# Kernel tuning notes

Measured on AMD Instinct MI355X. Metric: run time of the kernel, lower is better.

## Reference

```python
import jax, jax.numpy as jnp
import numpy as np

B, S, D, H, FFN = 8, 1024, 1024, 16, 4096
DH = D // H  # per-head dim = 64
NEG = -1e9
EPS = 1e-5


def layer_norm(x):
    # F.layer_norm over last dim, no affine params (matches add_and_norm_dropout)
    mu = jnp.mean(x, axis=-1, keepdims=True)
    var = jnp.var(x, axis=-1, keepdims=True)
    return (x - mu) / jnp.sqrt(var + EPS)


def setup_inputs() -> dict:
    key = jax.random.key(0)
    ks = jax.random.split(key, 10)
    scale = 1.0 / np.sqrt(D)
    x = jax.random.normal(ks[0], (B, S, D), dtype=jnp.float32)
    real_lengths = jax.random.randint(ks[1], (B,), 1, S + 1)
    # per-head projection weights stacked: [H, D, DH] (nn.Linear(D, DH, bias=False) per head)
    Wq = jax.random.uniform(ks[2], (H, D, DH), jnp.float32, -scale, scale)
    Wk = jax.random.uniform(ks[3], (H, D, DH), jnp.float32, -scale, scale)
    Wv = jax.random.uniform(ks[4], (H, D, DH), jnp.float32, -scale, scale)
    Wo = jax.random.uniform(ks[5], (D, H * DH), jnp.float32, -scale, scale)  # Linear(H*DH, D, bias=False)
    W1 = jax.random.uniform(ks[6], (FFN, D), jnp.float32, -scale, scale)
    b1 = jax.random.uniform(ks[7], (FFN,), jnp.float32, -scale, scale)
    s2 = 1.0 / np.sqrt(FFN)
    W2 = jax.random.uniform(ks[8], (D, FFN), jnp.float32, -s2, s2)
    b2 = jax.random.uniform(ks[9], (D,), jnp.float32, -s2, s2)
    return {"x": x, "real_lengths": real_lengths, "Wq": Wq, "Wk": Wk, "Wv": Wv,
            "Wo": Wo, "W1": W1, "b1": b1, "W2": W2, "b2": b2}


def reference(x, real_lengths, Wq, Wk, Wv, Wo, W1, b1, W2, b2):
    b, s, d = x.shape
    # padding mask: True where key position >= real_length (masked out)
    key_pad = jnp.arange(s)[None, :] >= real_lengths[:, None]  # [B, S]

    # batched per-head projections (equivalent to the Python per-head loop)
    q = jnp.einsum('bsd,hde->bhse', x, Wq)
    k = jnp.einsum('bsd,hde->bhse', x, Wk)
    v = jnp.einsum('bsd,hde->bhse', x, Wv)

    scores = jnp.einsum('bhse,bhte->bhst', q, k) / jnp.sqrt(jnp.float32(DH))
    scores = jnp.where(key_pad[:, None, None, :], NEG, scores)
    attn = jax.nn.softmax(scores, axis=-1)
    heads = jnp.einsum('bhst,bhte->bhse', attn, v)       # [B,H,S,DH]
    concat = heads.transpose(0, 2, 1, 3).reshape(b, s, d)  # head concat
    attn_out = concat @ Wo.T

    x1 = layer_norm(x + attn_out)  # add & norm (eval: no dropout)

    ffn = jax.nn.relu(x1 @ W1.T + b1) @ W2.T + b2
    return layer_norm(x1 + ffn)
```

## Files before the change

### kernel.cpp

```cpp
#include <hip/hip_runtime.h>
#include <hip/hip_bf16.h>
#include <math.h>

#define B_ 8
#define S_ 1024
#define D_ 1024
#define H_ 16
#define DH_ 64
#define FFN_ 4096
#define NEG_ (-1e9f)
#define EPS_ 1e-5f

typedef float f32x4 __attribute__((ext_vector_type(4)));
typedef short bf16x8 __attribute__((ext_vector_type(8)));

__device__ __forceinline__ ushort f2b(float f) {
  __hip_bfloat16 h = __float2bfloat16(f);
  return *reinterpret_cast<ushort*>(&h);
}
__device__ __forceinline__ float b2f(ushort u) {
  return __uint_as_float((unsigned)u << 16);
}

__device__ __forceinline__ void gload16(const void* g, void* l) {
  auto* lp = (__attribute__((address_space(3))) unsigned*)(uintptr_t)(l);
  __builtin_amdgcn_global_load_lds(
      (const __attribute__((address_space(1))) unsigned*)g, lp, 16, 0, 0);
}

__device__ __forceinline__ void* swz_ptr(void* base, int row, int col) {
  int byte = (row << 7) + (col << 1);
  byte ^= (row & 7) << 4;
  return (char*)base + byte;
}
__device__ __forceinline__ void* swz256(void* base, int row, int col) {
  int byte = (row << 8) + (col << 1);
  byte ^= (row & 7) << 4;
  return (char*)base + byte;
}

#define BARR asm volatile("s_barrier" ::: "memory")
#define LGKM0                                         \
  do {                                                \
    asm volatile("s_waitcnt lgkmcnt(0)" ::: "memory"); \
    __builtin_amdgcn_sched_barrier(0);                \
  } while (0)

__global__ __launch_bounds__(256) void prep_k(
    const float* __restrict__ x, const float* __restrict__ Wq,
    const float* __restrict__ Wk, const float* __restrict__ Wv,
    const float* __restrict__ Wo, const float* __restrict__ W1,
    const float* __restrict__ W2, ushort* __restrict__ xbf,
    ushort* __restrict__ qkvw, ushort* __restrict__ wob,
    ushort* __restrict__ w1b, ushort* __restrict__ w2b) {
  const int blk = blockIdx.x, t = threadIdx.x;
  if (blk < 8192) {
    int i = blk * 256 + t;
    float4 v = ((const float4*)x)[i];
    ushort4 o;
    o.x = f2b(v.x); o.y = f2b(v.y); o.z = f2b(v.z); o.w = f2b(v.w);
    ((ushort4*)xbf)[i] = o;
  } else if (blk < 8192 + 12288) {
    int idx = (blk - 8192) * 256 + t;
    int e = idx & 63, k = (idx >> 6) & 1023;
    int h = (idx >> 16) & 15, which = idx >> 20;
    const float* W = (which == 0) ? Wq : (which == 1 ? Wk : Wv);
    float v = W[((size_t)h * D_ + k) * DH_ + e];
    qkvw[((size_t)which * 1024 + h * 64 + e) * 1024 + k] = f2b(v);
  } else if (blk < 8192 + 12288 + 1024) {
    int i = (blk - 8192 - 12288) * 256 + t;
    float4 v = ((const float4*)Wo)[i];
    ushort4 o;
    o.x = f2b(v.x); o.y = f2b(v.y); o.z = f2b(v.z); o.w = f2b(v.w);
    ((ushort4*)wob)[i] = o;
  } else if (blk < 8192 + 12288 + 1024 + 4096) {
    int i = (blk - 8192 - 12288 - 1024) * 256 + t;
    float4 v = ((const float4*)W1)[i];
    ushort4 o;
    o.x = f2b(v.x); o.y = f2b(v.y); o.z = f2b(v.z); o.w = f2b(v.w);
    ((ushort4*)w1b)[i] = o;
  } else {
    int i = (blk - 8192 - 12288 - 1024 - 4096) * 256 + t;
    float4 v = ((const float4*)W2)[i];
    ushort4 o;
    o.x = f2b(v.x); o.y = f2b(v.y); o.z = f2b(v.z); o.w = f2b(v.w);
    ((ushort4*)w2b)[i] = o;
  }
}

template <int BIAS, int RELU, int VSPLIT>
__global__ __launch_bounds__(512, 2) void gemm8p(
    const ushort* __restrict__ A, const ushort* __restrict__ Bt,
    const float* __restrict__ bias, ushort* __restrict__ C,
    ushort* __restrict__ vT, int M, int N, int K) {
  __shared__ ushort lds[2][2][2][256 * 32];
  const int nbn = N >> 8;
  const int nwg = gridDim.x;
  const int cpx = nwg >> 3;
  const int bid = blockIdx.x;
  const int swz = (bid & 7) * cpx + (bid >> 3);
  const int bm = swz / nbn, bn = swz % nbn;

  const int t = threadIdx.x;
  const int lane = t & 63, lr = lane & 15, lg = lane >> 4;
  const int wid = t >> 6, wr = wid >> 2, wc = wid & 3;
  const size_t Kb = (size_t)K * 2;
  const char* Ab = (const char*)A + ((size_t)(bm << 8)) * Kb;
  const char* Bb = (const char*)Bt + ((size_t)(bn << 8)) * Kb;
  const int NT = K >> 6;
  const int niter = NT >> 1;

  const int g0row = t >> 2;
  const int gsi = (t & 3) ^ (g0row & 3);
  auto STG = [&](int mat, int kh, int kt) {
    char* base = (char*)&lds[kt & 1][mat][kh][0];
    const char* gsrc = mat ? Bb : Ab;
#pragma unroll
    for (int j = 0; j < 2; j++) {
      int row = g0row + j * 128;
      const char* src = gsrc + (size_t)row * Kb +
                        (size_t)(kt * 64 + kh * 32) * 2 + gsi * 16;
      gload16(src, base + t * 16 + j * 8192);
    }
  };

  const int rg = (lg ^ (lr & 3)) << 3;
#define LDA(DST, BUF, KH, QM)                                            \
  _Pragma("unroll") for (int mm = 0; mm < 4; mm++) {                     \
    int row = wr * 128 + (QM)*64 + mm * 16 + lr;                         \
    DST[mm] = *(const bf16x8*)&lds[BUF][0][KH][row * 32 + rg];           \
  }
#define LDB(DST, BUF, KH)                                                \
  _Pragma("unroll") for (int nn = 0; nn < 4; nn++) {                     \
    int row = wc * 64 + nn * 16 + lr;                                    \
    DST[nn] = *(const bf16x8*)&lds[BUF][1][KH][row * 32 + rg];           \
  }
#define MFQ(QM, AS, BS)                                                  \
  do {                                                                   \
    __builtin_amdgcn_s_setprio(1);                                       \
    _Pragma("unroll") for (int mm = 0; mm < 4; mm++)                     \
        _Pragma("unroll") for (int nn = 0; nn < 4; nn++)                 \
            acc[(QM)*4 + mm][nn] = __builtin_amdgcn_mfma_f32_16x16x32_bf16( \
                AS[mm], BS[nn], acc[(QM)*4 + mm][nn], 0, 0, 0);          \
    __builtin_amdgcn_s_setprio(0);                                       \
  } while (0)

  f32x4 acc[8][4] = {};
  bf16x8 aS0[4], aS1[4], bS0[4], bS1[4];

  STG(0, 0, 0); STG(1, 0, 0); STG(0, 1, 0); STG(1, 1, 0);
  STG(0, 0, 1); STG(1, 0, 1);
  asm volatile("s_waitcnt vmcnt(4)" ::: "memory");
  BARR;

  for (int i = 0; i < niter; i++) {
    const int c1 = 2 * i + 1, c2 = 2 * i + 2, c3 = 2 * i + 3;
    LDA(aS0, 0, 0, 0); LDB(bS0, 0, 0); STG(0, 1, c1);
    BARR; LGKM0; MFQ(0, aS0, bS0); BARR;
    LDA(aS1, 0, 0, 1); STG(1, 1, c1);
    BARR; LGKM0; MFQ(1, aS1, bS0); BARR;
    LDA(aS0, 0, 1, 0); LDB(bS1, 0, 1);
    if (c2 < NT) STG(0, 0, c2);
    BARR; LGKM0; MFQ(0, aS0, bS1); BARR;
    LDA(aS1, 0, 1, 1);
    if (c2 < NT) STG(1, 0, c2);
    BARR; LGKM0; MFQ(1, aS1, bS1);
    if (i + 1 < niter)
      asm volatile("s_waitcnt vmcnt(4)" ::: "memory");
    else
      asm volatile("s_waitcnt vmcnt(0)" ::: "memory");
    BARR;
    LDA(aS0, 1, 0, 0); LDB(bS0, 1, 0);
    if (c2 < NT) STG(0, 1, c2);
    BARR; LGKM0; MFQ(0, aS0, bS0); BARR;
    LDA(aS1, 1, 0, 1);
    if (c2 < NT) STG(1, 1, c2);
    BARR; LGKM0; MFQ(1, aS1, bS0); BARR;
    LDA(aS0, 1, 1, 0); LDB(bS1, 1, 1);
    if (c3 < NT) STG(0, 0, c3);
    BARR; LGKM0; MFQ(0, aS0, bS1); BARR;
    LDA(aS1, 1, 1, 1);
    if (c3 < NT) STG(1, 0, c3);
    BARR; LGKM0; MFQ(1, aS1, bS1);
    asm volatile("s_waitcnt vmcnt(4)" ::: "memory");
    BARR;
  }
#undef LDA
#undef LDB
#undef MFQ

  const int r0 = (bm << 8) + wr * 128 + lg * 4;
  const int c0 = (bn << 8) + wc * 64 + lr;
#pragma unroll
  for (int m = 0; m < 8; m++) {
#pragma unroll
    for (int n = 0; n < 4; n++) {
      int col = c0 + n * 16;
      float bv = BIAS ? bias[col] : 0.0f;
      if (VSPLIT && col >= 2048) {
        int row = r0 + m * 16;
        int hh = (col - 2048) >> 6, e = col & 63;
        ushort4 uv;
        uv.x = f2b(acc[m][n][0]); uv.y = f2b(acc[m][n][1]);
        uv.z = f2b(acc[m][n][2]); uv.w = f2b(acc[m][n][3]);
        *(ushort4*)&vT[((((size_t)(row >> 10) * 16 + hh) * 64 + e) << 10) +
                       (row & 1023)] = uv;
      } else {
#pragma unroll
        for (int q = 0; q < 4; q++) {
          int row = r0 + m * 16 + q;
          float v = acc[m][n][q] + bv;
          if (RELU) v = fmaxf(v, 0.0f);
          if (VSPLIT)
            C[(size_t)row * 2048 + col] = f2b(v);
          else
            C[(size_t)row * N + col] = f2b(v);
        }
      }
    }
  }
}

template <int BIAS, int RELU>
__global__ __launch_bounds__(256) void gemm_bf16(
    const ushort* __restrict__ A, const ushort* __restrict__ Bt,
    const float* __restrict__ bias, ushort* __restrict__ C,
    int M, int N, int K) {
  __shared__ ushort Al[2][128 * 64];
  __shared__ ushort Bl[2][128 * 64];
  const int nb = N >> 7;
  const int nwg = gridDim.x;
  const int cpx = nwg >> 3;
  const int bid = blockIdx.x;
  const int swb = (bid & 7) * cpx + (bid >> 3);
  const int bm = swb / nb, bn = swb % nb;
  const int t = threadIdx.x;
  const int lane = t & 63;
  const int wid = t >> 6, wr = wid >> 1, wc = wid & 1;
  const int row0 = bm << 7, col0 = bn << 7;
  const size_t Kb = (size_t)K * 2;
  const int NT = K >> 6;

  const char* Abase = (const char*)A + (size_t)row0 * Kb;
  const char* Bbase = (const char*)Bt + (size_t)col0 * Kb;

  f32x4 acc[4][4] = {};
  const int o0 = t * 16;
  const int lrow = lane & 15, lkb = (lane >> 4) * 8;

  auto STAGE = [&](int buf, int kt) {
#pragma unroll
    for (int i = 0; i < 4; i++) {
      int ob = o0 + i * 4096;
      int row = ob >> 7, inrow = ob & 127;
      const char* ga = Abase + (size_t)row * Kb + kt * 128 + inrow;
      const char* gb = Bbase + (size_t)row * Kb + kt * 128 + inrow;
      gload16(ga, (char*)&Al[buf][0] + ob);
      gload16(gb, (char*)&Bl[buf][0] + ob);
    }
  };
  auto COMPUTE = [&](int buf) {
#pragma unroll
    for (int kk = 0; kk < 64; kk += 32) {
      bf16x8 af[4], bfr[4];
      const int lk = lkb + kk;
#pragma unroll
      for (int m = 0; m < 4; m++)
        af[m] = *(const bf16x8*)&Al[buf][(wr * 64 + m * 16 + lrow) * 64 + lk];
#pragma unroll
      for (int n = 0; n < 4; n++)
        bfr[n] = *(const bf16x8*)&Bl[buf][(wc * 64 + n * 16 + lrow) * 64 + lk];
#pragma unroll
      for (int m = 0; m < 4; m++)
#pragma unroll
        for (int n = 0; n < 4; n++)
          acc[m][n] = __builtin_amdgcn_mfma_f32_16x16x32_bf16(
              af[m], bfr[n], acc[m][n], 0, 0, 0);
    }
  };

  STAGE(0, 0);
  __syncthreads();
  int cur = 0;
  for (int kt = 1; kt < NT; kt++) {
    STAGE(cur ^ 1, kt);
    COMPUTE(cur);
    __syncthreads();
    cur ^= 1;
  }
  COMPUTE(cur);

  const int rbase = row0 + wr * 64 + (lane >> 4) * 4;
  const int cbase = col0 + wc * 64 + (lane & 15);
#pragma unroll
  for (int m = 0; m < 4; m++) {
#pragma unroll
    for (int n = 0; n < 4; n++) {
      int col = cbase + n * 16;
      float bv = BIAS ? bias[col] : 0.0f;
#pragma unroll
      for (int q = 0; q < 4; q++) {
        int row = rbase + m * 16 + q;
        float v = acc[m][n][q] + bv;
        if (RELU) v = fmaxf(v, 0.0f);
        C[(size_t)row * N + col] = f2b(v);
      }
    }
  }
}

__global__ __launch_bounds__(256) void attention_mfma_k(
    const ushort* __restrict__ qk, const ushort* __restrict__ vT,
    const int* __restrict__ lens, ushort* __restrict__ concat) {
  __shared__ ushort Qs[64 * 64];
  __shared__ ushort Ks[128 * 64];
  __shared__ ushort Vt[64 * 128];
  __shared__ ushort Pl[4][16 * 128];
  const int blk = blockIdx.x;
  const int b = blk & 7, h = (blk >> 3) & 15, q0 = (blk >> 7) << 6;
  const int t = threadIdx.x;
  const int lane = t & 63, w = t >> 6;
  const int lr = lane & 15, lg = lane >> 4;
  const int lg4 = lg * 4;
  const int len_b = lens[b];
  ushort* Plw = &Pl[w][0];
  const ushort* vbase = vT + ((size_t)(b * 16 + h) << 16);

#pragma unroll
  for (int i = 0; i < 4; i++) {
    int idx = t + i * 256;
    int r = idx >> 4, eq = idx & 15;
    const ushort* src =
        qk + ((size_t)(b * S_ + q0 + r)) * 2048 + h * 64 + eq * 4;
    *(ushort4*)swz_ptr(Qs, r, eq * 4) = *(const ushort4*)src;
  }
  __syncthreads();
  bf16x8 qf[2];
#pragma unroll
  for (int ds = 0; ds < 2; ds++)
    qf[ds] = *(const bf16x8*)swz_ptr(Qs, w * 16 + lr, lg * 8 + ds * 32);

  float mrun = -INFINITY, lrun = 0.f;
  f32x4 o[4] = {};

  ushort4 kreg[8], vreg[8];
  auto LOADT = [&](int j0) {
#pragma unroll
    for (int i = 0; i < 8; i++) {
      int idx = t + i * 256;
      int kr = idx >> 4, keq = idx & 15;
      kreg[i] = *(const ushort4*)(qk + ((size_t)(b * S_ + j0 + kr)) * 2048 +
                                  1024 + h * 64 + keq * 4);
      int vr = idx >> 5, vc = idx & 31;
      vreg[i] = *(const ushort4*)(vbase + (size_t)vr * 1024 + j0 + vc * 4);
    }
  };

  const int ntiles = (len_b + 127) >> 7;
  LOADT(0);
  for (int jt = 0; jt < ntiles; jt++) {
    const int j0 = jt << 7;
    __syncthreads();
#pragma unroll
    for (int i = 0; i < 8; i++) {
      int idx = t + i * 256;
      int kr = idx >> 4, keq = idx & 15;
      *(ushort4*)swz_ptr(Ks, kr, keq * 4) = kreg[i];
      int vr = idx >> 5, vc = idx & 31;
      *(ushort4*)swz256(Vt, vr, vc * 4) = vreg[i];
    }
    if (jt + 1 < ntiles) LOADT(j0 + 128);
    __syncthreads();

    f32x4 sacc[8];
    __builtin_amdgcn_s_setprio(1);
#pragma unroll
    for (int mb = 0; mb < 8; mb++) {
      sacc[mb] = (f32x4){0.f, 0.f, 0.f, 0.f};
#pragma unroll
      for (int ds = 0; ds < 2; ds++) {
        bf16x8 kf = *(const bf16x8*)swz_ptr(Ks, mb * 16 + lr, lg * 8 + ds * 32);
        sacc[mb] = __builtin_amdgcn_mfma_f32_16x16x32_bf16(kf, qf[ds], sacc[mb],
                                                           0, 0, 0);
      }
    }
    __builtin_amdgcn_s_setprio(0);

    float p[8][4];
    float pmax = -INFINITY;
#pragma unroll
    for (int mb = 0; mb < 8; mb++)
#pragma unroll
      for (int qi = 0; qi < 4; qi++) {
        float v = sacc[mb][qi] * 0.125f;
        if (j0 + mb * 16 + lg4 + qi >= len_b) v = NEG_;
        p[mb][qi] = v;
        pmax = fmaxf(pmax, v);
      }
    pmax = fmaxf(pmax, __shfl_xor(pmax, 16));
    pmax = fmaxf(pmax, __shfl_xor(pmax, 32));
    if (!__all(pmax - mrun <= 8.0f)) {
      float mnew = fmaxf(mrun, pmax);
      float sc = __expf(mrun - mnew);
      mrun = mnew;
      lrun *= sc;
#pragma unroll
      for (int qi = 0; qi < 4; qi++) {
        float scq = __shfl(sc, (lg << 4) + lg4 + qi);
#pragma unroll
        for (int dt = 0; dt < 4; dt++) o[dt][qi] *= scq;
      }
    }
    float rs = 0.f;
#pragma unroll
    for (int mb = 0; mb < 8; mb++)
#pragma unroll
      for (int qi = 0; qi < 4; qi++) {
        float e = __expf(p[mb][qi] - mrun);
        p[mb][qi] = e;
        rs += e;
      }
    rs += __shfl_xor(rs, 16);
    rs += __shfl_xor(rs, 32);
    lrun += rs;

#pragma unroll
    for (int mb = 0; mb < 8; mb++) {
      ushort2 w0, w1;
      w0.x = f2b(p[mb][0]); w0.y = f2b(p[mb][1]);
      w1.x = f2b(p[mb][2]); w1.y = f2b(p[mb][3]);
      *(ushort2*)swz256(Plw, lr, mb * 16 + lg4) = w0;
      *(ushort2*)swz256(Plw, lr, mb * 16 + lg4 + 2) = w1;
    }

    bf16x8 pf[4];
#pragma unroll
    for (int ks = 0; ks < 4; ks++)
      pf[ks] = *(const bf16x8*)swz256(Plw, lr, lg * 8 + ks * 32);
    __builtin_amdgcn_s_setprio(1);
#pragma unroll
    for (int dt = 0; dt < 4; dt++) {
#pragma unroll
      for (int ks = 0; ks < 4; ks++) {
        bf16x8 vf =
            *(const bf16x8*)swz256(Vt, dt * 16 + lr, ks * 32 + lg * 8);
        o[dt] = __builtin_amdgcn_mfma_f32_16x16x32_bf16(pf[ks], vf, o[dt],
                                                        0, 0, 0);
      }
    }
    __builtin_amdgcn_s_setprio(0);
  }

#pragma unroll
  for (int qi = 0; qi < 4; qi++) {
    float lq = __shfl(lrun, (lg << 4) + lg4 + qi);
    float inv = 1.0f / lq;
    size_t row = (size_t)(b * S_ + q0 + w * 16 + lg4 + qi);
#pragma unroll
    for (int dt = 0; dt < 4; dt++)
      concat[row * 1024 + h * 64 + dt * 16 + lr] = f2b(o[dt][qi] * inv);
  }
}

template <int WBF>
__global__ __launch_bounds__(256) void add_ln_k(const float* __restrict__ a,
                                                const ushort* __restrict__ r,
                                                float* __restrict__ y,
                                                ushort* __restrict__ yb) {
  const int row = blockIdx.x, t = threadIdx.x;
  const float4 av = ((const float4*)(a + (size_t)row * 1024))[t];
  const ushort4 rv = ((const ushort4*)(r + (size_t)row * 1024))[t];
  float v[4] = {av.x + b2f(rv.x), av.y + b2f(rv.y), av.z + b2f(rv.z),
                av.w + b2f(rv.w)};
  float s = v[0] + v[1] + v[2] + v[3];
  float q = v[0] * v[0] + v[1] * v[1] + v[2] * v[2] + v[3] * v[3];
#pragma unroll
  for (int off = 1; off < 64; off <<= 1) {
    s += __shfl_xor(s, off);
    q += __shfl_xor(q, off);
  }
  __shared__ float ss[4], sq[4];
  int wave = t >> 6, lane = t & 63;
  if (lane == 0) { ss[wave] = s; sq[wave] = q; }
  __syncthreads();
  s = ss[0] + ss[1] + ss[2] + ss[3];
  q = sq[0] + sq[1] + sq[2] + sq[3];
  float mean = s * (1.f / 1024.f);
  float var = q * (1.f / 1024.f) - mean * mean;
  float inv = 1.0f / sqrtf(var + EPS_);
  float4 yo;
  yo.x = (v[0] - mean) * inv; yo.y = (v[1] - mean) * inv;
  yo.z = (v[2] - mean) * inv; yo.w = (v[3] - mean) * inv;
  ((float4*)(y + (size_t)row * 1024))[t] = yo;
  if (WBF) {
    ushort4 ob;
    ob.x = f2b(yo.x); ob.y = f2b(yo.y); ob.z = f2b(yo.z); ob.w = f2b(yo.w);
    ((ushort4*)(yb + (size_t)row * 1024))[t] = ob;
  }
}

extern "C" void kernel_launch(void* const* d_in, const int* in_sizes, int n_in,
                              void* d_out, int out_size, void* d_ws, size_t ws_size,
                              hipStream_t stream) {
  const float* x  = (const float*)d_in[0];
  const int* len  = (const int*)d_in[1];
  const float* Wq = (const float*)d_in[2];
  const float* Wk = (const float*)d_in[3];
  const float* Wv = (const float*)d_in[4];
  const float* Wo = (const float*)d_in[5];
  const float* W1 = (const float*)d_in[6];
  const float* b1 = (const float*)d_in[7];
  const float* W2 = (const float*)d_in[8];
  const float* b2 = (const float*)d_in[9];
  float* out = (float*)d_out;

  if (ws_size < (size_t)184 * 1024 * 1024) return;
  char* w = (char*)d_ws;
  ushort* xbf    = (ushort*)(w);
  ushort* qkvw   = (ushort*)(w + ((size_t)16 << 20));
  ushort* wob    = (ushort*)(w + ((size_t)22 << 20));
  ushort* w1b    = (ushort*)(w + ((size_t)24 << 20));
  ushort* w2b    = (ushort*)(w + ((size_t)32 << 20));
  ushort* qk2    = (ushort*)(w + ((size_t)40 << 20));
  ushort* vT     = (ushort*)(w + ((size_t)72 << 20));
  ushort* concat = (ushort*)(w + ((size_t)88 << 20));
  ushort* attno  = (ushort*)(w + ((size_t)104 << 20));
  float*  x1     = (float*) (w + ((size_t)136 << 20));
  ushort* x1b    = (ushort*)(w + ((size_t)168 << 20));
  ushort* hidden = (ushort*)(w + ((size_t)40 << 20));
  ushort* ffn2o  = (ushort*)(w + ((size_t)104 << 20));

  prep_k<<<29696, 256, 0, stream>>>(x, Wq, Wk, Wv, Wo, W1, W2,
                                    xbf, qkvw, wob, w1b, w2b);

  gemm8p<0, 0, 1><<<32 * 12, 512, 0, stream>>>(xbf, qkvw, nullptr, qk2,
                                               vT, 8192, 3072, 1024);
  attention_mfma_k<<<2048, 256, 0, stream>>>(qk2, vT, len, concat);
  gemm_bf16<0, 0><<<64 * 8, 256, 0, stream>>>(concat, wob, nullptr, attno,
                                              8192, 1024, 1024);
  add_ln_k<1><<<8192, 256, 0, stream>>>(x, attno, x1, x1b);
  gemm8p<1, 1, 0><<<32 * 16, 512, 0, stream>>>(x1b, w1b, b1, hidden,
                                               nullptr, 8192, 4096, 1024);
  gemm_bf16<1, 0><<<64 * 8, 256, 0, stream>>>(hidden, w2b, b2, ffn2o,
                                              8192, 1024, 4096);
  add_ln_k<0><<<8192, 256, 0, stream>>>(x1, ffn2o, out, nullptr);
}
```

Baseline: 390.5 us.

## Replace 128-tile N=1024 GEMMs with split-K 256-tile gemm8p, reduce in add+LN

The two N=1024 GEMMs (output projection and FFN down-projection) move from the simpler 128x128 double-buffered kernel to the tuned 256x256 8-wave gemm8p kernel. Split-K by two keeps the grid at 256 workgroups. Each half writes a bf16 partial, and the add+layernorm kernel now sums both partials. This aims for better MFMA efficiency and data reuse, at the cost of extra partial-result traffic and an extra bf16 rounding of each partial.

New measurement: 382.0 us. -2.2%, faster.

```diff
diff --git a/kernel.cpp b/kernel.cpp
--- a/kernel.cpp
+++ b/kernel.cpp
@@ -88,26 +88,35 @@
   }
 }
 
-template <int BIAS, int RELU, int VSPLIT>
+template <int BIAS, int RELU, int VSPLIT, int SPLITK>
 __global__ __launch_bounds__(512, 2) void gemm8p(
     const ushort* __restrict__ A, const ushort* __restrict__ Bt,
     const float* __restrict__ bias, ushort* __restrict__ C,
-    ushort* __restrict__ vT, int M, int N, int K) {
+    ushort* __restrict__ C2, int M, int N, int K) {
   __shared__ ushort lds[2][2][2][256 * 32];
+  int bid = blockIdx.x;
+  int nwg = gridDim.x;
+  int kh2 = 0;
+  if (SPLITK) {
+    int hw = nwg >> 1;
+    if (bid >= hw) { kh2 = 1; bid -= hw; }
+    nwg = hw;
+  }
   const int nbn = N >> 8;
-  const int nwg = gridDim.x;
   const int cpx = nwg >> 3;
-  const int bid = blockIdx.x;
   const int swz = (bid & 7) * cpx + (bid >> 3);
   const int bm = swz / nbn, bn = swz % nbn;
+  const int Keff = SPLITK ? (K >> 1) : K;
 
   const int t = threadIdx.x;
   const int lane = t & 63, lr = lane & 15, lg = lane >> 4;
   const int wid = t >> 6, wr = wid >> 2, wc = wid & 3;
   const size_t Kb = (size_t)K * 2;
-  const char* Ab = (const char*)A + ((size_t)(bm << 8)) * Kb;
-  const char* Bb = (const char*)Bt + ((size_t)(bn << 8)) * Kb;
-  const int NT = K >> 6;
+  const char* Ab = (const char*)A + ((size_t)(bm << 8)) * Kb +
+                   (size_t)kh2 * Keff * 2;
+  const char* Bb = (const char*)Bt + ((size_t)(bn << 8)) * Kb +
+                   (size_t)kh2 * Keff * 2;
+  const int NT = Keff >> 6;
   const int niter = NT >> 1;
 
   const int g0row = t >> 2;
@@ -189,6 +198,8 @@
 #undef LDB
 #undef MFQ
 
+  ushort* Cout = (SPLITK && kh2) ? C2 : C;
+  const int addb = BIAS && !(SPLITK && kh2);
   const int r0 = (bm << 8) + wr * 128 + lg * 4;
   const int c0 = (bn << 8) + wc * 64 + lr;
 #pragma unroll
@@ -196,14 +207,14 @@
 #pragma unroll
     for (int n = 0; n < 4; n++) {
       int col = c0 + n * 16;
-      float bv = BIAS ? bias[col] : 0.0f;
+      float bv = addb ? bias[col] : 0.0f;
       if (VSPLIT && col >= 2048) {
         int row = r0 + m * 16;
         int hh = (col - 2048) >> 6, e = col & 63;
         ushort4 uv;
         uv.x = f2b(acc[m][n][0]); uv.y = f2b(acc[m][n][1]);
         uv.z = f2b(acc[m][n][2]); uv.w = f2b(acc[m][n][3]);
-        *(ushort4*)&vT[((((size_t)(row >> 10) * 16 + hh) * 64 + e) << 10) +
+        *(ushort4*)&C2[((((size_t)(row >> 10) * 16 + hh) * 64 + e) << 10) +
                        (row & 1023)] = uv;
       } else {
 #pragma unroll
@@ -212,98 +223,10 @@
           float v = acc[m][n][q] + bv;
           if (RELU) v = fmaxf(v, 0.0f);
           if (VSPLIT)
-            C[(size_t)row * 2048 + col] = f2b(v);
+            Cout[(size_t)row * 2048 + col] = f2b(v);
           else
-            C[(size_t)row * N + col] = f2b(v);
+            Cout[(size_t)row * N + col] = f2b(v);
         }
-      }
-    }
-  }
-}
-
-template <int BIAS, int RELU>
-__global__ __launch_bounds__(256) void gemm_bf16(
-    const ushort* __restrict__ A, const ushort* __restrict__ Bt,
-    const float* __restrict__ bias, ushort* __restrict__ C,
-    int M, int N, int K) {
-  __shared__ ushort Al[2][128 * 64];
-  __shared__ ushort Bl[2][128 * 64];
-  const int nb = N >> 7;
-  const int nwg = gridDim.x;
-  const int cpx = nwg >> 3;
-  const int bid = blockIdx.x;
-  const int swb = (bid & 7) * cpx + (bid >> 3);
-  const int bm = swb / nb, bn = swb % nb;
-  const int t = threadIdx.x;
-  const int lane = t & 63;
-  const int wid = t >> 6, wr = wid >> 1, wc = wid & 1;
-  const int row0 = bm << 7, col0 = bn << 7;
-  const size_t Kb = (size_t)K * 2;
-  const int NT = K >> 6;
-
-  const char* Abase = (const char*)A + (size_t)row0 * Kb;
-  const char* Bbase = (const char*)Bt + (size_t)col0 * Kb;
-
-  f32x4 acc[4][4] = {};
-  const int o0 = t * 16;
-  const int lrow = lane & 15, lkb = (lane >> 4) * 8;
-
-  auto STAGE = [&](int buf, int kt) {
-#pragma unroll
-    for (int i = 0; i < 4; i++) {
-      int ob = o0 + i * 4096;
-      int row = ob >> 7, inrow = ob & 127;
-      const char* ga = Abase + (size_t)row * Kb + kt * 128 + inrow;
-      const char* gb = Bbase + (size_t)row * Kb + kt * 128 + inrow;
-      gload16(ga, (char*)&Al[buf][0] + ob);
-      gload16(gb, (char*)&Bl[buf][0] + ob);
-    }
-  };
-  auto COMPUTE = [&](int buf) {
-#pragma unroll
-    for (int kk = 0; kk < 64; kk += 32) {
-      bf16x8 af[4], bfr[4];
-      const int lk = lkb + kk;
-#pragma unroll
-      for (int m = 0; m < 4; m++)
-        af[m] = *(const bf16x8*)&Al[buf][(wr * 64 + m * 16 + lrow) * 64 + lk];
-#pragma unroll
-      for (int n = 0; n < 4; n++)
-        bfr[n] = *(const bf16x8*)&Bl[buf][(wc * 64 + n * 16 + lrow) * 64 + lk];
-#pragma unroll
-      for (int m = 0; m < 4; m++)
-#pragma unroll
-        for (int n = 0; n < 4; n++)
-          acc[m][n] = __builtin_amdgcn_mfma_f32_16x16x32_bf16(
-              af[m], bfr[n], acc[m][n], 0, 0, 0);
-    }
-  };
-
-  STAGE(0, 0);
-  __syncthreads();
-  int cur = 0;
-  for (int kt = 1; kt < NT; kt++) {
-    STAGE(cur ^ 1, kt);
-    COMPUTE(cur);
-    __syncthreads();
-    cur ^= 1;
-  }
-  COMPUTE(cur);
-
-  const int rbase = row0 + wr * 64 + (lane >> 4) * 4;
-  const int cbase = col0 + wc * 64 + (lane & 15);
-#pragma unroll
-  for (int m = 0; m < 4; m++) {
-#pragma unroll
-    for (int n = 0; n < 4; n++) {
-      int col = cbase + n * 16;
-      float bv = BIAS ? bias[col] : 0.0f;
-#pragma unroll
-      for (int q = 0; q < 4; q++) {
-        int row = rbase + m * 16 + q;
-        float v = acc[m][n][q] + bv;
-        if (RELU) v = fmaxf(v, 0.0f);
-        C[(size_t)row * N + col] = f2b(v);
       }
     }
   }
@@ -462,9 +385,10 @@
   }
 }
 
-template <int WBF>
+template <int WBF, int TWO>
 __global__ __launch_bounds__(256) void add_ln_k(const float* __restrict__ a,
                                                 const ushort* __restrict__ r,
+                                                const ushort* __restrict__ r2,
                                                 float* __restrict__ y,
                                                 ushort* __restrict__ yb) {
   const int row = blockIdx.x, t = threadIdx.x;
@@ -472,6 +396,11 @@
   const ushort4 rv = ((const ushort4*)(r + (size_t)row * 1024))[t];
   float v[4] = {av.x + b2f(rv.x), av.y + b2f(rv.y), av.z + b2f(rv.z),
                 av.w + b2f(rv.w)};
+  if (TWO) {
+    const ushort4 r2v = ((const ushort4*)(r2 + (size_t)row * 1024))[t];
+    v[0] += b2f(r2v.x); v[1] += b2f(r2v.y);
+    v[2] += b2f(r2v.z); v[3] += b2f(r2v.w);
+  }
   float s = v[0] + v[1] + v[2] + v[3];
   float q = v[0] * v[0] + v[1] * v[1] + v[2] * v[2] + v[3] * v[3];
 #pragma unroll
@@ -524,24 +453,24 @@
   ushort* qk2    = (ushort*)(w + ((size_t)40 << 20));
   ushort* vT     = (ushort*)(w + ((size_t)72 << 20));
   ushort* concat = (ushort*)(w + ((size_t)88 << 20));
-  ushort* attno  = (ushort*)(w + ((size_t)104 << 20));
+  ushort* parta  = (ushort*)(w + ((size_t)104 << 20));
+  ushort* partb  = (ushort*)(w + ((size_t)120 << 20));
   float*  x1     = (float*) (w + ((size_t)136 << 20));
   ushort* x1b    = (ushort*)(w + ((size_t)168 << 20));
   ushort* hidden = (ushort*)(w + ((size_t)40 << 20));
-  ushort* ffn2o  = (ushort*)(w + ((size_t)104 << 20));
 
   prep_k<<<29696, 256, 0, stream>>>(x, Wq, Wk, Wv, Wo, W1, W2,
                                     xbf, qkvw, wob, w1b, w2b);
 
-  gemm8p<0, 0, 1><<<32 * 12, 512, 0, stream>>>(xbf, qkvw, nullptr, qk2,
-                                               vT, 8192, 3072, 1024);
+  gemm8p<0, 0, 1, 0><<<32 * 12, 512, 0, stream>>>(xbf, qkvw, nullptr, qk2,
+                                                  vT, 8192, 3072, 1024);
   attention_mfma_k<<<2048, 256, 0, stream>>>(qk2, vT, len, concat);
-  gemm_bf16<0, 0><<<64 * 8, 256, 0, stream>>>(concat, wob, nullptr, attno,
-                                              8192, 1024, 1024);
-  add_ln_k<1><<<8192, 256, 0, stream>>>(x, attno, x1, x1b);
-  gemm8p<1, 1, 0><<<32 * 16, 512, 0, stream>>>(x1b, w1b, b1, hidden,
-                                               nullptr, 8192, 4096, 1024);
-  gemm_bf16<1, 0><<<64 * 8, 256, 0, stream>>>(hidden, w2b, b2, ffn2o,
-                                              8192, 1024, 4096);
-  add_ln_k<0><<<8192, 256, 0, stream>>>(x1, ffn2o, out, nullptr);
-}
+  gemm8p<0, 0, 0, 1><<<256, 512, 0, stream>>>(concat, wob, nullptr, parta,
+                                              partb, 8192, 1024, 1024);
+  add_ln_k<1, 1><<<8192, 256, 0, stream>>>(x, parta, partb, x1, x1b);
+  gemm8p<1, 1, 0, 0><<<32 * 16, 512, 0, stream>>>(x1b, w1b, b1, hidden,
+                                                  nullptr, 8192, 4096, 1024);
+  gemm8p<1, 0, 0, 1><<<256, 512, 0, stream>>>(hidden, w2b, b2, parta,
+                                              partb, 8192, 1024, 4096);
+  add_ln_k<0, 1><<<8192, 256, 0, stream>>>(x1, parta, partb, out, nullptr);
+}
```
